# Performance work log

Measured on AMD Instinct MI355X. Metric: run time of the kernel, lower is better.

Reference implementation:

```python
import jax, jax.numpy as jnp
import numpy as np
import math

B, T, D, H = 4, 1024, 512, 8
DH = D // H


def setup_inputs() -> dict:
    key = jax.random.key(0)
    ks = jax.random.split(key, 8)
    s = 1.0 / math.sqrt(D)
    return {
        "x": jax.random.normal(ks[0], (B, T, D), jnp.float32),
        "Wq_w": jax.random.normal(ks[1], (D, D), jnp.float32) * s,
        "Wq_b": jnp.zeros((D,), jnp.float32),
        "Wk_w": jax.random.normal(ks[2], (D, D), jnp.float32) * s,
        "Wk_b": jnp.zeros((D,), jnp.float32),
        "Wv_w": jax.random.normal(ks[3], (D, D), jnp.float32) * s,
        "Wv_b": jnp.zeros((D,), jnp.float32),
        "Ws_w": jax.random.normal(ks[4], (D, H), jnp.float32) * s,
        "Ws_b": jnp.zeros((H,), jnp.float32),
        "Wo_w": jax.random.normal(ks[5], (D, D), jnp.float32) * s,
        "Wo_b": jnp.zeros((D,), jnp.float32),
    }


def reference(x, Wq_w, Wq_b, Wk_w, Wk_b, Wv_w, Wv_b, Ws_w, Ws_b, Wo_w, Wo_b):
    b, t, d = x.shape
    # projections (weights stored [in, out]; same math as torch Linear)
    q = (x @ Wq_w + Wq_b).reshape(b, t, H, DH).transpose(0, 2, 1, 3)  # [B,H,T,dh]
    k = (x @ Wk_w + Wk_b).reshape(b, t, H, DH).transpose(0, 2, 1, 3)
    v = (x @ Wv_w + Wv_b).reshape(b, t, H, DH).transpose(0, 2, 1, 3)

    logits = jnp.einsum("bhtd,bhsd->bhts", q, k) / math.sqrt(DH)
    series = jax.nn.softmax(logits, axis=-1)  # [B,H,T,T] (dropout p=0 -> no-op)

    sigma = jax.nn.softplus(x @ Ws_w + Ws_b).transpose(0, 2, 1) + 1e-6  # [B,H,T]

    idx = jnp.arange(t, dtype=jnp.float32)
    dist2 = (idx[None, :] - idx[:, None]) ** 2  # [T,T]
    s2 = sigma[..., None] ** 2 + 1e-6           # [B,H,T,1]
    prior = jnp.exp(-dist2[None, None] / (2.0 * s2))
    prior = prior / (prior.sum(axis=-1, keepdims=True) + 1e-9)

    out = jnp.einsum("bhts,bhsd->bhtd", series, v)
    out = out.transpose(0, 2, 1, 3).reshape(b, t, d)
    out = out @ Wo_w + Wo_b
    return out, series, prior, sigma
```

## Files before the change

kernel.cpp:

```cpp
#include <hip/hip_runtime.h>
#include <math.h>

#define BB 4
#define TT 1024
#define DD 512
#define HH 8
#define DHH 64

typedef short bf8_t __attribute__((ext_vector_type(8)));
typedef float f32x4 __attribute__((ext_vector_type(4)));

__device__ __forceinline__ float softplus_f(float z) {
    return fmaxf(z, 0.f) + log1pf(__expf(-fabsf(z)));
}

__device__ __forceinline__ unsigned short f2bf(float f) {
    union { float f; unsigned int u; } v; v.f = f;
    return (unsigned short)((v.u + 0x7FFFu + ((v.u >> 16) & 1u)) >> 16);
}

__global__ __launch_bounds__(256) void cast_x_kernel(
    const float* __restrict__ x, unsigned short* __restrict__ xbf)
{
    int i = blockIdx.x * 256 + threadIdx.x;
    float4 a = *(const float4*)&x[(size_t)i * 8];
    float4 b = *(const float4*)&x[(size_t)i * 8 + 4];
    union { unsigned short u[8]; int4 v; } o;
    o.u[0] = f2bf(a.x); o.u[1] = f2bf(a.y); o.u[2] = f2bf(a.z); o.u[3] = f2bf(a.w);
    o.u[4] = f2bf(b.x); o.u[5] = f2bf(b.y); o.u[6] = f2bf(b.z); o.u[7] = f2bf(b.w);
    *(int4*)&xbf[(size_t)i * 8] = o.v;
}

__global__ __launch_bounds__(256) void transpose_w_kernel(
    const float* __restrict__ Wq, const float* __restrict__ Wk,
    const float* __restrict__ Wv, const float* __restrict__ Wo,
    unsigned short* __restrict__ wt, unsigned short* __restrict__ woT)
{
    __shared__ float tile[32][33];
    const int tid = threadIdx.x;
    const int z = blockIdx.z;
    const float* W = (z == 0) ? Wq : (z == 1) ? Wk : (z == 2) ? Wv : Wo;
    unsigned short* dst = (z < 3) ? (wt + (size_t)z * 512 * 512) : woT;
    const int k0 = blockIdx.x * 32, n0 = blockIdx.y * 32;
    const int ty = tid >> 3, tx = tid & 7;

    float4 v = *(const float4*)&W[(size_t)(k0 + ty) * 512 + n0 + tx * 4];
    tile[ty][tx*4+0] = v.x; tile[ty][tx*4+1] = v.y;
    tile[ty][tx*4+2] = v.z; tile[ty][tx*4+3] = v.w;
    __syncthreads();
    ushort4 o;
    o.x = f2bf(tile[tx*4+0][ty]);
    o.y = f2bf(tile[tx*4+1][ty]);
    o.z = f2bf(tile[tx*4+2][ty]);
    o.w = f2bf(tile[tx*4+3][ty]);
    *(ushort4*)&dst[(size_t)(n0 + ty) * 512 + k0 + tx * 4] = o;
}

__global__ __launch_bounds__(256) void transpose_ws_kernel(
    const float* __restrict__ Ws, unsigned short* __restrict__ wt)
{
    const int tid = threadIdx.x;
    #pragma unroll
    for (int i = 0; i < 16; ++i) {
        int idx = i * 256 + tid;
        int k = idx >> 3, n = idx & 7;
        wt[(size_t)(1536 + n) * 512 + k] = f2bf(Ws[idx]);
    }
}

__global__ __launch_bounds__(256) void proj_mfma_kernel(
    const unsigned short* __restrict__ xbf,
    const unsigned short* __restrict__ wt,
    const float* __restrict__ bq, const float* __restrict__ bk,
    const float* __restrict__ bv, const float* __restrict__ bs,
    unsigned short* __restrict__ qbf, unsigned short* __restrict__ kbf,
    unsigned short* __restrict__ vbf, float* __restrict__ sigma_out)
{
    __shared__ unsigned short a_s[64][64];
    __shared__ unsigned short b_s[64][64];
    const int tid = threadIdx.x;
    const int w = tid >> 6, l = tid & 63, lr = l & 15, lg = l >> 4;
    const int ct = blockIdx.x;
    const int m0 = blockIdx.y * 64;
    const int n0 = ct * 64;

    f32x4 acc[4];
    #pragma unroll
    for (int nb = 0; nb < 4; ++nb) acc[nb] = (f32x4){0.f, 0.f, 0.f, 0.f};

    for (int k0 = 0; k0 < 512; k0 += 64) {
        __syncthreads();
        #pragma unroll
        for (int rep = 0; rep < 2; ++rep) {
            int idx = rep * 256 + tid;
            int row = idx >> 3, cg = idx & 7;
            *(int4*)&a_s[row][(cg ^ (row & 7)) * 8] =
                *(const int4*)&xbf[(size_t)(m0 + row) * 512 + k0 + cg * 8];
            *(int4*)&b_s[row][(cg ^ (row & 7)) * 8] =
                *(const int4*)&wt[(size_t)(n0 + row) * 512 + k0 + cg * 8];
        }
        __syncthreads();
        #pragma unroll
        for (int ks = 0; ks < 2; ++ks) {
            int arow = w * 16 + lr;
            bf8_t af = *(const bf8_t*)&a_s[arow][((ks*4 + lg) ^ (arow & 7)) * 8];
            #pragma unroll
            for (int nb = 0; nb < 4; ++nb) {
                int brow = nb * 16 + lr;
                bf8_t bf = *(const bf8_t*)&b_s[brow][((ks*4 + lg) ^ (brow & 7)) * 8];
                acc[nb] = __builtin_amdgcn_mfma_f32_16x16x32_bf16(af, bf, acc[nb], 0, 0, 0);
            }
        }
    }

    if (ct < 24) {
        const int seg = ct >> 3;
        const int h = ct & 7;
        const float* bias = (seg == 0) ? bq : (seg == 1) ? bk : bv;
        unsigned short* dst = (seg == 0) ? qbf : (seg == 1) ? kbf : vbf;
        const float sc = (seg == 0) ? 0.125f : 1.f;
        #pragma unroll
        for (int nb = 0; nb < 4; ++nb) {
            float bb = bias[h * 64 + nb * 16 + lr];
            #pragma unroll
            for (int r = 0; r < 4; ++r) {
                int m = m0 + w * 16 + lg * 4 + r;
                int b = m >> 10, t = m & 1023;
                dst[((size_t)((b*HH + h)*TT + t)) * 64 + nb * 16 + lr] =
                    f2bf((acc[nb][r] + bb) * sc);
            }
        }
    } else if (lr < 8) {
        float bb = bs[lr];
        #pragma unroll
        for (int r = 0; r < 4; ++r) {
            int m = m0 + w * 16 + lg * 4 + r;
            int b = m >> 10, t = m & 1023;
            sigma_out[(size_t)(b*HH + lr)*TT + t] = softplus_f(acc[0][r] + bb) + 1e-6f;
        }
    }
}

__global__ __launch_bounds__(256) void attn_kernel(
    const unsigned short* __restrict__ qbf,
    const unsigned short* __restrict__ kbf,
    const unsigned short* __restrict__ vbf,
    float* __restrict__ series, unsigned short* __restrict__ obf)
{
    __shared__ unsigned short k_lds[64][72];
    __shared__ unsigned short v_lds[64][64];
    __shared__ unsigned short p_lds[4][16][72];

    const int tid = threadIdx.x;
    const int w  = tid >> 6, l = tid & 63;
    const int lr = l & 15,  lg = l >> 4;
    const int bh = blockIdx.y;
    const int qr = blockIdx.x * 64 + w * 16;

    bf8_t aq[2];
    {
        const unsigned short* qrow = &qbf[((size_t)bh * TT + qr + lr) * 64];
        aq[0] = *(const bf8_t*)&qrow[lg * 8];
        aq[1] = *(const bf8_t*)&qrow[32 + lg * 8];
    }

    float psum[4] = {0.f, 0.f, 0.f, 0.f};
    for (int st = 0; st < 16; ++st) {
        __syncthreads();
        #pragma unroll
        for (int rep = 0; rep < 2; ++rep) {
            int idx = rep * 256 + tid;
            int tr = idx >> 3, cg = idx & 7;
            *(int4*)&k_lds[tr][cg * 8] =
                *(const int4*)&kbf[((size_t)bh * TT + st * 64 + tr) * 64 + cg * 8];
        }
        __syncthreads();
        #pragma unroll
        for (int nb = 0; nb < 4; ++nb) {
            f32x4 acc = {0.f, 0.f, 0.f, 0.f};
            #pragma unroll
            for (int c = 0; c < 2; ++c) {
                bf8_t bk = *(const bf8_t*)&k_lds[nb * 16 + lr][c * 32 + lg * 8];
                acc = __builtin_amdgcn_mfma_f32_16x16x32_bf16(aq[c], bk, acc, 0, 0, 0);
            }
            #pragma unroll
            for (int r = 0; r < 4; ++r) psum[r] += __expf(acc[r]);
        }
    }
    #pragma unroll
    for (int r = 0; r < 4; ++r) {
        psum[r] += __shfl_xor(psum[r], 1);
        psum[r] += __shfl_xor(psum[r], 2);
        psum[r] += __shfl_xor(psum[r], 4);
        psum[r] += __shfl_xor(psum[r], 8);
    }
    float inv[4];
    #pragma unroll
    for (int r = 0; r < 4; ++r) inv[r] = 1.f / psum[r];

    f32x4 oacc[4];
    #pragma unroll
    for (int nb = 0; nb < 4; ++nb) oacc[nb] = (f32x4){0.f, 0.f, 0.f, 0.f};

    for (int st = 0; st < 16; ++st) {
        __syncthreads();
        #pragma unroll
        for (int rep = 0; rep < 2; ++rep) {
            int idx = rep * 256 + tid;
            int tr = idx >> 3, cg = idx & 7;
            *(int4*)&k_lds[tr][cg * 8] =
                *(const int4*)&kbf[((size_t)bh * TT + st * 64 + tr) * 64 + cg * 8];
        }
        #pragma unroll
        for (int rep = 0; rep < 2; ++rep) {
            int idx = rep * 256 + tid;
            int sr = idx >> 3, cg = idx & 7;
            int4 vv = *(const int4*)&vbf[((size_t)bh * TT + st * 64 + sr) * 64 + cg * 8];
            const unsigned short* pv = (const unsigned short*)&vv;
            #pragma unroll
            for (int j = 0; j < 8; ++j) {
                int row = cg * 8 + j;
                int gsw = ((sr >> 3) ^ j ^ cg) & 7;
                v_lds[row][gsw * 8 + (sr & 7)] = pv[j];
            }
        }
        __syncthreads();

        #pragma unroll
        for (int nb = 0; nb < 4; ++nb) {
            f32x4 acc = {0.f, 0.f, 0.f, 0.f};
            #pragma unroll
            for (int c = 0; c < 2; ++c) {
                bf8_t bk = *(const bf8_t*)&k_lds[nb * 16 + lr][c * 32 + lg * 8];
                acc = __builtin_amdgcn_mfma_f32_16x16x32_bf16(aq[c], bk, acc, 0, 0, 0);
            }
            #pragma unroll
            for (int r = 0; r < 4; ++r) {
                float e = __expf(acc[r]);
                series[((size_t)bh * TT + qr + lg * 4 + r) * TT + st * 64 + nb * 16 + lr]
                    = e * inv[r];
                p_lds[w][lg * 4 + r][nb * 16 + lr] = f2bf(e);
            }
        }

        bf8_t pa0 = *(const bf8_t*)&p_lds[w][lr][lg * 8];
        bf8_t pa1 = *(const bf8_t*)&p_lds[w][lr][32 + lg * 8];
        #pragma unroll
        for (int nb = 0; nb < 4; ++nb) {
            #pragma unroll
            for (int c = 0; c < 2; ++c) {
                int row = nb * 16 + lr;
                int gsw = ((c * 4 + lg) ^ (row & 7) ^ (row >> 3)) & 7;
                bf8_t bv = *(const bf8_t*)&v_lds[row][gsw * 8];
                oacc[nb] = __builtin_amdgcn_mfma_f32_16x16x32_bf16(
                    (c == 0) ? pa0 : pa1, bv, oacc[nb], 0, 0, 0);
            }
        }
    }

    const int b = bh >> 3, h = bh & 7;
    #pragma unroll
    for (int nb = 0; nb < 4; ++nb)
        #pragma unroll
        for (int r = 0; r < 4; ++r) {
            int t = qr + lg * 4 + r;
            obf[((size_t)(b * TT + t)) * 512 + h * 64 + nb * 16 + lr] =
                f2bf(oacc[nb][r] * inv[r]);
        }
}

__global__ __launch_bounds__(256) void outproj_mfma_kernel(
    const unsigned short* __restrict__ obf,
    const unsigned short* __restrict__ woT,
    const float* __restrict__ bo, float* __restrict__ out)
{
    __shared__ unsigned short a_s[64][64];
    __shared__ unsigned short b_s[64][64];
    const int tid = threadIdx.x;
    const int w = tid >> 6, l = tid & 63, lr = l & 15, lg = l >> 4;
    const int n0 = blockIdx.x * 64;
    const int m0 = blockIdx.y * 64;

    f32x4 acc[4];
    #pragma unroll
    for (int nb = 0; nb < 4; ++nb) acc[nb] = (f32x4){0.f, 0.f, 0.f, 0.f};

    for (int k0 = 0; k0 < 512; k0 += 64) {
        __syncthreads();
        #pragma unroll
        for (int rep = 0; rep < 2; ++rep) {
            int idx = rep * 256 + tid;
            int row = idx >> 3, cg = idx & 7;
            *(int4*)&a_s[row][(cg ^ (row & 7)) * 8] =
                *(const int4*)&obf[(size_t)(m0 + row) * 512 + k0 + cg * 8];
            *(int4*)&b_s[row][(cg ^ (row & 7)) * 8] =
                *(const int4*)&woT[(size_t)(n0 + row) * 512 + k0 + cg * 8];
        }
        __syncthreads();
        #pragma unroll
        for (int ks = 0; ks < 2; ++ks) {
            int arow = w * 16 + lr;
            bf8_t af = *(const bf8_t*)&a_s[arow][((ks*4 + lg) ^ (arow & 7)) * 8];
            #pragma unroll
            for (int nb = 0; nb < 4; ++nb) {
                int brow = nb * 16 + lr;
                bf8_t bf = *(const bf8_t*)&b_s[brow][((ks*4 + lg) ^ (brow & 7)) * 8];
                acc[nb] = __builtin_amdgcn_mfma_f32_16x16x32_bf16(af, bf, acc[nb], 0, 0, 0);
            }
        }
    }

    #pragma unroll
    for (int nb = 0; nb < 4; ++nb) {
        float bb = bo[n0 + nb * 16 + lr];
        #pragma unroll
        for (int r = 0; r < 4; ++r) {
            int m = m0 + w * 16 + lg * 4 + r;
            out[(size_t)m * 512 + n0 + nb * 16 + lr] = acc[nb][r] + bb;
        }
    }
}

__global__ __launch_bounds__(256) void prior_kernel(
    const float* __restrict__ sigma, float* __restrict__ prior)
{
    const int tid = threadIdx.x;
    const int w = tid >> 6, tc = tid & 63;
    const int row = blockIdx.x * 4 + w;
    const int t = row & 1023;

    float sg = sigma[row];
    float c = 1.f / (2.f * (sg*sg + 1e-6f));

    float e[16]; float sum = 0.f;
    #pragma unroll
    for (int j = 0; j < 16; ++j) {
        int s = j*64 + tc;
        float d = (float)(t - s);
        e[j] = __expf(-(d*d) * c);
        sum += e[j];
    }
    sum += __shfl_xor(sum, 32);
    sum += __shfl_xor(sum, 16);
    sum += __shfl_xor(sum, 8);
    sum += __shfl_xor(sum, 4);
    sum += __shfl_xor(sum, 2);
    sum += __shfl_xor(sum, 1);
    float inv = 1.f / (sum + 1e-9f);

    float* pr = prior + (size_t)row * 1024;
    #pragma unroll
    for (int j = 0; j < 16; ++j) pr[j*64 + tc] = e[j] * inv;
}

extern "C" void kernel_launch(void* const* d_in, const int* in_sizes, int n_in,
                              void* d_out, int out_size, void* d_ws, size_t ws_size,
                              hipStream_t stream)
{
    const float* x    = (const float*)d_in[0];
    const float* Wq_w = (const float*)d_in[1];
    const float* Wq_b = (const float*)d_in[2];
    const float* Wk_w = (const float*)d_in[3];
    const float* Wk_b = (const float*)d_in[4];
    const float* Wv_w = (const float*)d_in[5];
    const float* Wv_b = (const float*)d_in[6];
    const float* Ws_w = (const float*)d_in[7];
    const float* Ws_b = (const float*)d_in[8];
    const float* Wo_w = (const float*)d_in[9];
    const float* Wo_b = (const float*)d_in[10];

    float* out    = (float*)d_out;
    float* series = out + (size_t)BB*TT*DD;
    float* prior  = series + (size_t)BB*HH*TT*TT;
    float* sigma  = prior + (size_t)BB*HH*TT*TT;

    const size_t nx = (size_t)BB*TT*DD;
    unsigned short* xbf = (unsigned short*)d_ws;
    unsigned short* wt  = xbf + nx;
    unsigned short* woT = wt + (size_t)1600*512;
    unsigned short* qbf = woT + (size_t)512*512;
    unsigned short* kbf = qbf + nx;
    unsigned short* vbf = kbf + nx;
    unsigned short* obf = vbf + nx;

    cast_x_kernel<<<1024, 256, 0, stream>>>(x, xbf);
    transpose_w_kernel<<<dim3(16, 16, 4), 256, 0, stream>>>(
        Wq_w, Wk_w, Wv_w, Wo_w, wt, woT);
    transpose_ws_kernel<<<1, 256, 0, stream>>>(Ws_w, wt);

    proj_mfma_kernel<<<dim3(25, 64), 256, 0, stream>>>(
        xbf, wt, Wq_b, Wk_b, Wv_b, Ws_b, qbf, kbf, vbf, sigma);

    attn_kernel<<<dim3(16, 32), 256, 0, stream>>>(qbf, kbf, vbf, series, obf);

    outproj_mfma_kernel<<<dim3(8, 64), 256, 0, stream>>>(obf, woT, Wo_b, out);

    prior_kernel<<<8192, 256, 0, stream>>>(sigma, prior);
}
```

Measured before the change: 122.7 us.

## Fuse Gaussian prior computation into attention kernel loop

```diff
diff --git a/kernel.cpp b/kernel.cpp
--- a/kernel.cpp
+++ b/kernel.cpp
@@ -145,7 +145,9 @@
     const unsigned short* __restrict__ qbf,
     const unsigned short* __restrict__ kbf,
     const unsigned short* __restrict__ vbf,
-    float* __restrict__ series, unsigned short* __restrict__ obf)
+    const float* __restrict__ sigma,
+    float* __restrict__ series, float* __restrict__ prior,
+    unsigned short* __restrict__ obf)
 {
     __shared__ unsigned short k_lds[64][72];
     __shared__ unsigned short v_lds[64][64];
@@ -256,6 +258,29 @@
                     (c == 0) ? pa0 : pa1, bv, oacc[nb], 0, 0, 0);
             }
         }
+
+        {
+            int t = qr + st;
+            float sg = sigma[(size_t)bh * TT + t];
+            float cc = 1.f / (2.f * (sg * sg + 1e-6f));
+            float e[16]; float sum = 0.f;
+            #pragma unroll
+            for (int j = 0; j < 16; ++j) {
+                float d = (float)(t - (j * 64 + l));
+                e[j] = __expf(-(d * d) * cc);
+                sum += e[j];
+            }
+            sum += __shfl_xor(sum, 32);
+            sum += __shfl_xor(sum, 16);
+            sum += __shfl_xor(sum, 8);
+            sum += __shfl_xor(sum, 4);
+            sum += __shfl_xor(sum, 2);
+            sum += __shfl_xor(sum, 1);
+            float pinv = 1.f / (sum + 1e-9f);
+            float* pr = prior + ((size_t)bh * TT + t) * TT;
+            #pragma unroll
+            for (int j = 0; j < 16; ++j) pr[j * 64 + l] = e[j] * pinv;
+        }
     }
 
     const int b = bh >> 3, h = bh & 7;
@@ -319,38 +344,6 @@
             out[(size_t)m * 512 + n0 + nb * 16 + lr] = acc[nb][r] + bb;
         }
     }
-}
-
-__global__ __launch_bounds__(256) void prior_kernel(
-    const float* __restrict__ sigma, float* __restrict__ prior)
-{
-    const int tid = threadIdx.x;
-    const int w = tid >> 6, tc = tid & 63;
-    const int row = blockIdx.x * 4 + w;
-    const int t = row & 1023;
-
-    float sg = sigma[row];
-    float c = 1.f / (2.f * (sg*sg + 1e-6f));
-
-    float e[16]; float sum = 0.f;
-    #pragma unroll
-    for (int j = 0; j < 16; ++j) {
-        int s = j*64 + tc;
-        float d = (float)(t - s);
-        e[j] = __expf(-(d*d) * c);
-        sum += e[j];
-    }
-    sum += __shfl_xor(sum, 32);
-    sum += __shfl_xor(sum, 16);
-    sum += __shfl_xor(sum, 8);
-    sum += __shfl_xor(sum, 4);
-    sum += __shfl_xor(sum, 2);
-    sum += __shfl_xor(sum, 1);
-    float inv = 1.f / (sum + 1e-9f);
-
-    float* pr = prior + (size_t)row * 1024;
-    #pragma unroll
-    for (int j = 0; j < 16; ++j) pr[j*64 + tc] = e[j] * inv;
 }
 
 extern "C" void kernel_launch(void* const* d_in, const int* in_sizes, int n_in,
@@ -391,9 +384,8 @@
     proj_mfma_kernel<<<dim3(25, 64), 256, 0, stream>>>(
         xbf, wt, Wq_b, Wk_b, Wv_b, Ws_b, qbf, kbf, vbf, sigma);
 
-    attn_kernel<<<dim3(16, 32), 256, 0, stream>>>(qbf, kbf, vbf, series, obf);
+    attn_kernel<<<dim3(16, 32), 256, 0, stream>>>(
+        qbf, kbf, vbf, sigma, series, prior, obf);
 
     outproj_mfma_kernel<<<dim3(8, 64), 256, 0, stream>>>(obf, woT, Wo_b, out);
-
-    prior_kernel<<<8192, 256, 0, stream>>>(sigma, prior);
-}
+}
```

New measurement: 117.6 us. 1.04x faster.
